# Performance work log

Measured on AMD Instinct MI355X. Metric: run time of the kernel, lower is better.

The kernel has to match this reference:

```python
import jax, jax.numpy as jnp
import numpy as np

B, K, D = 8, 1024, 512
H, DQ, DV = 8, 64, 64


def setup_inputs() -> dict:
    key = jax.random.key(0)
    ks = jax.random.split(key, 11)
    s = 0.02  # param init scale
    return {
        "query": jax.random.normal(ks[0], (B, K, D), jnp.float32),
        "key": jax.random.normal(ks[1], (B, K, D), jnp.float32),
        "value": jax.random.normal(ks[2], (B, K, D), jnp.float32),
        "Wq": jax.random.normal(ks[3], (D, H * DQ), jnp.float32) * s,
        "bq": jax.random.normal(ks[4], (H * DQ,), jnp.float32) * s,
        "Wk": jax.random.normal(ks[5], (D, H * DQ), jnp.float32) * s,
        "bk": jax.random.normal(ks[6], (H * DQ,), jnp.float32) * s,
        "Wv": jax.random.normal(ks[7], (D, H * DV), jnp.float32) * s,
        "bv": jax.random.normal(ks[8], (H * DV,), jnp.float32) * s,
        "Wo": jax.random.normal(ks[9], (H * DV, D), jnp.float32) * s,
        "bo": jax.random.normal(ks[10], (D,), jnp.float32) * s,
    }


def reference(query, key, value, Wq, bq, Wk, bk, Wv, bv, Wo, bo):
    b, k, _ = query.shape
    # Linear projections, split into heads: chunk(h, dim=-1) + cat(dim=0)
    # is equivalent to reshape (b, k, h, d) with head on a separate axis.
    q = (query @ Wq + bq).reshape(b, k, H, DQ)  # b k h dq
    kk = (key @ Wk + bk).reshape(b, k, H, DQ)   # b k h dq
    v = (value @ Wv + bv).reshape(b, k, H, DV)  # b k h dv
    # NOTE: original scales by sqrt(K) (sequence length), not sqrt(dq).
    scale = 1.0 / jnp.sqrt(jnp.asarray(k, q.dtype))
    scores = jnp.einsum("bqhd,bkhd->bhqk", q, kk) * scale
    attn = jax.nn.softmax(scores, axis=-1)
    ctx = jnp.einsum("bhqk,bkhd->bqhd", attn, v).reshape(b, k, H * DV)
    return ctx @ Wo + bo
```

## Files before the change

### kernel.cpp

```cpp
#include <hip/hip_runtime.h>
#include <hip/hip_bf16.h>

#define DEVI __device__ __forceinline__

typedef __attribute__((ext_vector_type(4))) float f32x4;
typedef __attribute__((ext_vector_type(8))) short bf16x8;

static constexpr int BB  = 8;
static constexpr int SEQ = 1024;
static constexpr int DIM = 512;
static constexpr int NH  = 8;
static constexpr int HD  = 64;
static constexpr int M   = BB * SEQ;


DEVI unsigned short f2bf(float x) {
  unsigned int u = __builtin_bit_cast(unsigned int, x);
  u += 0x7fffu + ((u >> 16) & 1u);
  return (unsigned short)(u >> 16);
}

DEVI float fexp2(float x) {
#if __has_builtin(__builtin_amdgcn_exp2f)
  return __builtin_amdgcn_exp2f(x);
#else
  float r; asm("v_exp_f32 %0, %1" : "=v"(r) : "v"(x)); return r;
#endif
}

DEVI void gload_lds16(const unsigned short* g, unsigned short* l) {
  __builtin_amdgcn_global_load_lds(
      (const __attribute__((address_space(1))) void*)g,
      (__attribute__((address_space(3))) void*)l, 16, 0, 0);
}


__global__ __launch_bounds__(256) void cvt3_kernel(const float* __restrict__ a,
                                                   const float* __restrict__ b,
                                                   const float* __restrict__ c,
                                                   unsigned short* __restrict__ oa,
                                                   unsigned short* __restrict__ ob,
                                                   unsigned short* __restrict__ oc) {
  const float* in = (blockIdx.y == 0) ? a : ((blockIdx.y == 1) ? b : c);
  unsigned short* out = (blockIdx.y == 0) ? oa : ((blockIdx.y == 1) ? ob : oc);
  int i = (blockIdx.x * 256 + threadIdx.x) * 4;
  float4 v = *reinterpret_cast<const float4*>(in + i);
  ushort4 o;
  o.x = f2bf(v.x); o.y = f2bf(v.y); o.z = f2bf(v.z); o.w = f2bf(v.w);
  *reinterpret_cast<ushort4*>(out + i) = o;
}


__global__ __launch_bounds__(256) void cvt_t4_kernel(const float* __restrict__ w0,
                                                     const float* __restrict__ w1,
                                                     const float* __restrict__ w2,
                                                     const float* __restrict__ w3,
                                                     unsigned short* __restrict__ o0,
                                                     unsigned short* __restrict__ o1,
                                                     unsigned short* __restrict__ o2,
                                                     unsigned short* __restrict__ o3) {
  const float* in = (blockIdx.z == 0) ? w0 : ((blockIdx.z == 1) ? w1 : ((blockIdx.z == 2) ? w2 : w3));
  unsigned short* out = (blockIdx.z == 0) ? o0 : ((blockIdx.z == 1) ? o1 : ((blockIdx.z == 2) ? o2 : o3));
  __shared__ float tile[32][33];
  int n0 = blockIdx.x * 32, k0 = blockIdx.y * 32;
  int tx = threadIdx.x & 31, ty = threadIdx.x >> 5;
#pragma unroll
  for (int r = 0; r < 32; r += 8)
    tile[ty + r][tx] = in[(size_t)(k0 + ty + r) * DIM + n0 + tx];
  __syncthreads();
#pragma unroll
  for (int r = 0; r < 32; r += 8)
    out[(size_t)(n0 + ty + r) * DIM + k0 + tx] = f2bf(tile[tx][ty + r]);
}


__global__ __launch_bounds__(256) void gemm_proj(const unsigned short* __restrict__ Aq,
                                                 const unsigned short* __restrict__ Ak,
                                                 const unsigned short* __restrict__ Av,
                                                 const unsigned short* __restrict__ WqT,
                                                 const unsigned short* __restrict__ WkT,
                                                 const unsigned short* __restrict__ WvT,
                                                 const float* __restrict__ bq,
                                                 const float* __restrict__ bk,
                                                 const float* __restrict__ bv,
                                                 unsigned short* __restrict__ qb,
                                                 unsigned short* __restrict__ kb,
                                                 unsigned short* __restrict__ vT,
                                                 float qscale) {
  __shared__ unsigned short smem[17408];
  unsigned short* lA = smem;
  unsigned short* lB = smem + 8192;

  const int z = blockIdx.z;
  const unsigned short* A = (z == 0) ? Aq : ((z == 1) ? Ak : Av);
  const unsigned short* Bt = (z == 0) ? WqT : ((z == 1) ? WkT : WvT);
  const float* bias = (z == 0) ? bq : ((z == 1) ? bk : bv);
  const float gs = (z == 0) ? qscale : 1.0f;

  const int tid = threadIdx.x;
  const int lane = tid & 63, wave = tid >> 6;
  const int wr = wave >> 1, wc = wave & 1;
  const int row0 = blockIdx.x * 128, col0 = blockIdx.y * 128;
  const int lr = lane & 15, lg = lane >> 4;

  f32x4 acc[4][4] = {};

  const int s0a = wave * 64;
  const int sA = s0a + lane, rA = sA >> 2, koA = (sA & 3) * 8;
  const int s0b = 256 + wave * 64;
  const int sB = s0b + lane, rB = sB >> 2, koB = (sB & 3) * 8;

#define GEMM_STAGE(buf, k0)                                                              \
  do {                                                                                   \
    gload_lds16(A + (size_t)(row0 + rA) * DIM + (k0) + koA, &lA[(buf)*4096 + s0a * 8]);  \
    gload_lds16(Bt + (size_t)(col0 + rA) * DIM + (k0) + koA, &lB[(buf)*4096 + s0a * 8]); \
    gload_lds16(A + (size_t)(row0 + rB) * DIM + (k0) + koB, &lA[(buf)*4096 + s0b * 8]);  \
    gload_lds16(Bt + (size_t)(col0 + rB) * DIM + (k0) + koB, &lB[(buf)*4096 + s0b * 8]); \
  } while (0)

  GEMM_STAGE(0, 0);
  __syncthreads();

  constexpr int NT = DIM / 32;
  for (int t = 0; t < NT; ++t) {
    const int cur = t & 1;
    if (t + 1 < NT) GEMM_STAGE(cur ^ 1, (t + 1) * 32);

    bf16x8 af[4], bfr[4];
#pragma unroll
    for (int m = 0; m < 4; ++m)
      af[m] = *reinterpret_cast<const bf16x8*>(&lA[cur * 4096 + (wr * 64 + m * 16 + lr) * 32 + lg * 8]);
#pragma unroll
    for (int n = 0; n < 4; ++n)
      bfr[n] = *reinterpret_cast<const bf16x8*>(&lB[cur * 4096 + (wc * 64 + n * 16 + lr) * 32 + lg * 8]);
    __builtin_amdgcn_s_setprio(1);
#pragma unroll
    for (int m = 0; m < 4; ++m)
#pragma unroll
      for (int n = 0; n < 4; ++n)
        acc[m][n] = __builtin_amdgcn_mfma_f32_16x16x32_bf16(af[m], bfr[n], acc[m][n], 0, 0, 0);
    __builtin_amdgcn_s_setprio(0);

    __syncthreads();
  }
#undef GEMM_STAGE

  if (z < 2) {
    unsigned short* C = (z == 0) ? qb : kb;
#pragma unroll
    for (int m = 0; m < 4; ++m) {
#pragma unroll
      for (int n = 0; n < 4; ++n) {
        int col = col0 + wc * 64 + n * 16 + lr;
        int r0 = row0 + wr * 64 + m * 16 + lg * 4;
        float bvv = bias[col];
#pragma unroll
        for (int j = 0; j < 4; ++j)
          C[(size_t)(r0 + j) * DIM + col] = f2bf((acc[m][n][j] + bvv) * gs);
      }
    }
  } else {
    unsigned short* ldsT = smem;
#pragma unroll
    for (int m = 0; m < 4; ++m) {
#pragma unroll
      for (int n = 0; n < 4; ++n) {
        const int col = wc * 64 + n * 16 + lr;
        const int r0l = wr * 64 + m * 16 + lg * 4;
        const float bvv = bias[col0 + col];
        ushort4 pk;
        pk.x = f2bf(acc[m][n][0] + bvv);
        pk.y = f2bf(acc[m][n][1] + bvv);
        pk.z = f2bf(acc[m][n][2] + bvv);
        pk.w = f2bf(acc[m][n][3] + bvv);
        *reinterpret_cast<ushort4*>(&ldsT[col * 136 + r0l]) = pk;
      }
    }
    __syncthreads();
    const int b = row0 >> 10, s_loc0 = row0 & 1023;
#pragma unroll
    for (int it = 0; it < 8; ++it) {
      int idx = it * 256 + tid;
      int c = idx >> 4, s8 = idx & 15;
      bf16x8 v = *reinterpret_cast<const bf16x8*>(&ldsT[c * 136 + s8 * 8]);
      *reinterpret_cast<bf16x8*>(
          vT + ((size_t)(b * DIM) + col0 + c) * SEQ + s_loc0 + s8 * 8) = v;
    }
  }
}


__global__ __launch_bounds__(256) void gemm_out(const unsigned short* __restrict__ A,
                                                const unsigned short* __restrict__ Bt,
                                                const float* __restrict__ bias,
                                                float* __restrict__ C) {
  __shared__ unsigned short lA[2][128 * 32];
  __shared__ unsigned short lB[2][128 * 32];
  const int tid = threadIdx.x;
  const int lane = tid & 63, wave = tid >> 6;
  const int wr = wave >> 1, wc = wave & 1;
  const int row0 = blockIdx.x * 128, col0 = blockIdx.y * 128;
  const int lr = lane & 15, lg = lane >> 4;

  f32x4 acc[4][4] = {};

  const int s0a = wave * 64;
  const int sA = s0a + lane, rA = sA >> 2, koA = (sA & 3) * 8;
  const int s0b = 256 + wave * 64;
  const int sB = s0b + lane, rB = sB >> 2, koB = (sB & 3) * 8;

#define GEMM_STAGE(buf, k0)                                                        \
  do {                                                                             \
    gload_lds16(A + (size_t)(row0 + rA) * DIM + (k0) + koA, &lA[buf][s0a * 8]);    \
    gload_lds16(Bt + (size_t)(col0 + rA) * DIM + (k0) + koA, &lB[buf][s0a * 8]);   \
    gload_lds16(A + (size_t)(row0 + rB) * DIM + (k0) + koB, &lA[buf][s0b * 8]);    \
    gload_lds16(Bt + (size_t)(col0 + rB) * DIM + (k0) + koB, &lB[buf][s0b * 8]);   \
  } while (0)

  GEMM_STAGE(0, 0);
  __syncthreads();

  constexpr int NT = DIM / 32;
  for (int t = 0; t < NT; ++t) {
    const int cur = t & 1;
    if (t + 1 < NT) GEMM_STAGE(cur ^ 1, (t + 1) * 32);

    bf16x8 af[4], bfr[4];
#pragma unroll
    for (int m = 0; m < 4; ++m)
      af[m] = *reinterpret_cast<const bf16x8*>(&lA[cur][(wr * 64 + m * 16 + lr) * 32 + lg * 8]);
#pragma unroll
    for (int n = 0; n < 4; ++n)
      bfr[n] = *reinterpret_cast<const bf16x8*>(&lB[cur][(wc * 64 + n * 16 + lr) * 32 + lg * 8]);
    __builtin_amdgcn_s_setprio(1);
#pragma unroll
    for (int m = 0; m < 4; ++m)
#pragma unroll
      for (int n = 0; n < 4; ++n)
        acc[m][n] = __builtin_amdgcn_mfma_f32_16x16x32_bf16(af[m], bfr[n], acc[m][n], 0, 0, 0);
    __builtin_amdgcn_s_setprio(0);

    __syncthreads();
  }
#undef GEMM_STAGE

#pragma unroll
  for (int m = 0; m < 4; ++m) {
#pragma unroll
    for (int n = 0; n < 4; ++n) {
      int col = col0 + wc * 64 + n * 16 + lr;
      int r0 = row0 + wr * 64 + m * 16 + lg * 4;
      float bv = bias[col];
#pragma unroll
      for (int j = 0; j < 4; ++j)
        C[(size_t)(r0 + j) * DIM + col] = acc[m][n][j] + bv;
    }
  }
}


__global__ __launch_bounds__(512) void attn_kernel(const unsigned short* __restrict__ qb,
                                                   const unsigned short* __restrict__ kb,
                                                   const unsigned short* __restrict__ vT,
                                                   unsigned short* __restrict__ ctx) {
  __shared__ unsigned short lK[2][64 * 64];
  __shared__ unsigned short lV[2][64 * 64];
  __shared__ unsigned short Pl[8][16 * 72];

  const int b = blockIdx.z, h = blockIdx.y;
  const int tid = threadIdx.x, lane = tid & 63, wave = tid >> 6;
  const int lr = lane & 15, lg = lane >> 4;
  const int q0 = blockIdx.x * 128 + wave * 16;

  const int sr = tid >> 3, sc = (tid & 7) ^ (sr & 7);
  const unsigned short* Kbase = kb + ((size_t)b * SEQ) * DIM + (size_t)h * HD;
  const unsigned short* Vbase = vT + (size_t)(b * NH + h) * HD * SEQ;

  bf16x8 qf0, qf1;
  {
    const unsigned short* qrow = qb + ((size_t)(b * SEQ) + q0 + lr) * DIM + h * HD;
    qf0 = *reinterpret_cast<const bf16x8*>(qrow + lg * 8);
    qf1 = *reinterpret_cast<const bf16x8*>(qrow + 32 + lg * 8);
  }

  float l_r[4] = {0.f, 0.f, 0.f, 0.f};
  f32x4 o_acc[4];
#pragma unroll
  for (int n = 0; n < 4; ++n) o_acc[n] = f32x4{0.f, 0.f, 0.f, 0.f};

  unsigned short* pw = Pl[wave];

  gload_lds16(Kbase + (size_t)sr * DIM + sc * 8, &lK[0][(wave * 64) * 8]);
  gload_lds16(Vbase + (size_t)sr * SEQ + sc * 8, &lV[0][(wave * 64) * 8]);
  __syncthreads();

  for (int t = 0; t < SEQ / 64; ++t) {
    const int cur = t & 1;
    if (t + 1 < SEQ / 64) {
      const int nk = (t + 1) * 64;
      gload_lds16(Kbase + (size_t)(nk + sr) * DIM + sc * 8, &lK[cur ^ 1][(wave * 64) * 8]);
      gload_lds16(Vbase + (size_t)sr * SEQ + nk + sc * 8, &lV[cur ^ 1][(wave * 64) * 8]);
    }

    f32x4 st[4];
    __builtin_amdgcn_s_setprio(1);
#pragma unroll
    for (int kt = 0; kt < 4; ++kt) {
      const int row = kt * 16 + lr;
      const char* rbase = (const char*)&lK[cur][0] + row * 128;
      const int sw = (row & 7) << 4;
      bf16x8 kf0 = *reinterpret_cast<const bf16x8*>(rbase + ((lg * 16) ^ sw));
      bf16x8 kf1 = *reinterpret_cast<const bf16x8*>(rbase + ((64 + lg * 16) ^ sw));
      f32x4 a = {};
      a = __builtin_amdgcn_mfma_f32_16x16x32_bf16(qf0, kf0, a, 0, 0, 0);
      a = __builtin_amdgcn_mfma_f32_16x16x32_bf16(qf1, kf1, a, 0, 0, 0);
      st[kt] = a;
    }
    __builtin_amdgcn_s_setprio(0);

#pragma unroll
    for (int j = 0; j < 4; ++j) {
      float p0 = fexp2(st[0][j]);
      float p1 = fexp2(st[1][j]);
      float p2 = fexp2(st[2][j]);
      float p3 = fexp2(st[3][j]);
      l_r[j] += (p0 + p1) + (p2 + p3);
      const int qrow = (lg * 4 + j) * 72;
      pw[qrow + lr] = f2bf(p0);
      pw[qrow + 16 + lr] = f2bf(p1);
      pw[qrow + 32 + lr] = f2bf(p2);
      pw[qrow + 48 + lr] = f2bf(p3);
    }

#pragma unroll
    for (int c = 0; c < 2; ++c) {
      bf16x8 pf = *reinterpret_cast<const bf16x8*>((const char*)pw + lr * 144 + c * 64 + lg * 16);
      __builtin_amdgcn_s_setprio(1);
#pragma unroll
      for (int n = 0; n < 4; ++n) {
        const int row = n * 16 + lr;
        bf16x8 vf = *reinterpret_cast<const bf16x8*>(
            (const char*)&lV[cur][0] + row * 128 + ((c * 64 + lg * 16) ^ ((row & 7) << 4)));
        o_acc[n] = __builtin_amdgcn_mfma_f32_16x16x32_bf16(pf, vf, o_acc[n], 0, 0, 0);
      }
      __builtin_amdgcn_s_setprio(0);
    }

    __syncthreads();
  }

  float invl[4];
#pragma unroll
  for (int j = 0; j < 4; ++j) {
    float l = l_r[j];
#pragma unroll
    for (int msk = 1; msk < 16; msk <<= 1) l += __shfl_xor(l, msk);
    invl[j] = 1.f / l;
  }
#pragma unroll
  for (int n = 0; n < 4; ++n)
#pragma unroll
    for (int j = 0; j < 4; ++j)
      pw[(lg * 4 + j) * 72 + n * 16 + lr] = f2bf(o_acc[n][j] * invl[j]);

#pragma unroll
  for (int it = 0; it < 2; ++it) {
    int idx = it * 64 + lane;
    int r = idx >> 3, cc = idx & 7;
    bf16x8 v = *reinterpret_cast<const bf16x8*>((const char*)pw + r * 144 + cc * 16);
    *reinterpret_cast<bf16x8*>(ctx + ((size_t)(b * SEQ) + q0 + r) * DIM + h * HD + cc * 8) = v;
  }
}


extern "C" void kernel_launch(void* const* d_in, const int* in_sizes, int n_in,
                              void* d_out, int out_size, void* d_ws, size_t ws_size,
                              hipStream_t stream) {
  const float* query = (const float*)d_in[0];
  const float* key_  = (const float*)d_in[1];
  const float* value = (const float*)d_in[2];
  const float* Wq = (const float*)d_in[3];
  const float* bq = (const float*)d_in[4];
  const float* Wk = (const float*)d_in[5];
  const float* bk = (const float*)d_in[6];
  const float* Wv = (const float*)d_in[7];
  const float* bv = (const float*)d_in[8];
  const float* Wo = (const float*)d_in[9];
  const float* bo = (const float*)d_in[10];
  float* out = (float*)d_out;

  unsigned short* ws = (unsigned short*)d_ws;
  const size_t NM = (size_t)M * DIM;
  const size_t NW = (size_t)DIM * DIM;
  unsigned short* xq   = ws;
  unsigned short* xk   = xq + NM;
  unsigned short* xv   = xk + NM;
  unsigned short* qb   = xv + NM;
  unsigned short* kbuf = qb + NM;
  unsigned short* vTb  = kbuf + NM;
  unsigned short* ctx  = vTb + NM;
  unsigned short* Wqt  = ctx + NM;
  unsigned short* Wkt  = Wqt + NW;
  unsigned short* Wvt  = Wkt + NW;
  unsigned short* Wot  = Wvt + NW;

  cvt3_kernel<<<dim3((int)(NM / 1024), 3), 256, 0, stream>>>(query, key_, value, xq, xk, xv);
  cvt_t4_kernel<<<dim3(16, 16, 4), 256, 0, stream>>>(Wq, Wk, Wv, Wo, Wqt, Wkt, Wvt, Wot);

  const float qscale = 0.03125f * 1.4426950408889634f;
  gemm_proj<<<dim3(M / 128, DIM / 128, 3), 256, 0, stream>>>(
      xq, xk, xv, Wqt, Wkt, Wvt, bq, bk, bv, qb, kbuf, vTb, qscale);

  attn_kernel<<<dim3(SEQ / 128, NH, BB), 512, 0, stream>>>(qb, kbuf, vTb, ctx);

  gemm_out<<<dim3(M / 128, DIM / 128), 256, 0, stream>>>(ctx, Wot, bo, out);
}
```

Before: 86.22 us.

## Triple-buffer LDS tiles in projection and output GEMMs with explicit vmcnt waits

Both GEMM kernels move from double-buffered to triple-buffered LDS staging. Loads run two k-tiles ahead, and explicit s_waitcnt vmcnt counts replace the full __syncthreads drain. The intent is to hide more global-load latency behind MFMA work. In exchange each block uses more shared memory, which may lower occupancy, and each step now has two barriers.

New measurement: 81.37 us. 1.06x faster.

```diff
diff --git a/kernel.cpp b/kernel.cpp
--- a/kernel.cpp
+++ b/kernel.cpp
@@ -87,9 +87,9 @@
                                                  unsigned short* __restrict__ kb,
                                                  unsigned short* __restrict__ vT,
                                                  float qscale) {
-  __shared__ unsigned short smem[17408];
+  __shared__ unsigned short smem[24576];
   unsigned short* lA = smem;
-  unsigned short* lB = smem + 8192;
+  unsigned short* lB = smem + 12288;
 
   const int z = blockIdx.z;
   const unsigned short* A = (z == 0) ? Aq : ((z == 1) ? Ak : Av);
@@ -118,32 +118,39 @@
     gload_lds16(Bt + (size_t)(col0 + rB) * DIM + (k0) + koB, &lB[(buf)*4096 + s0b * 8]); \
   } while (0)
 
+#define GEMM_STEP(cur, VMC)                                                              \
+  do {                                                                                   \
+    asm volatile("s_waitcnt vmcnt(" #VMC ")" ::: "memory");                              \
+    __builtin_amdgcn_s_barrier();                                                        \
+    bf16x8 af[4], bfr[4];                                                                \
+    _Pragma("unroll")                                                                    \
+    for (int m = 0; m < 4; ++m)                                                          \
+      af[m] = *reinterpret_cast<const bf16x8*>(&lA[(cur)*4096 + (wr * 64 + m * 16 + lr) * 32 + lg * 8]); \
+    _Pragma("unroll")                                                                    \
+    for (int n = 0; n < 4; ++n)                                                          \
+      bfr[n] = *reinterpret_cast<const bf16x8*>(&lB[(cur)*4096 + (wc * 64 + n * 16 + lr) * 32 + lg * 8]); \
+    __builtin_amdgcn_s_setprio(1);                                                       \
+    _Pragma("unroll")                                                                    \
+    for (int m = 0; m < 4; ++m)                                                          \
+      _Pragma("unroll")                                                                  \
+      for (int n = 0; n < 4; ++n)                                                        \
+        acc[m][n] = __builtin_amdgcn_mfma_f32_16x16x32_bf16(af[m], bfr[n], acc[m][n], 0, 0, 0); \
+    __builtin_amdgcn_s_setprio(0);                                                       \
+    asm volatile("" ::: "memory");                                                       \
+    __builtin_amdgcn_s_barrier();                                                        \
+  } while (0)
+
+  constexpr int NT = DIM / 32;
   GEMM_STAGE(0, 0);
-  __syncthreads();
-
-  constexpr int NT = DIM / 32;
-  for (int t = 0; t < NT; ++t) {
-    const int cur = t & 1;
-    if (t + 1 < NT) GEMM_STAGE(cur ^ 1, (t + 1) * 32);
-
-    bf16x8 af[4], bfr[4];
-#pragma unroll
-    for (int m = 0; m < 4; ++m)
-      af[m] = *reinterpret_cast<const bf16x8*>(&lA[cur * 4096 + (wr * 64 + m * 16 + lr) * 32 + lg * 8]);
-#pragma unroll
-    for (int n = 0; n < 4; ++n)
-      bfr[n] = *reinterpret_cast<const bf16x8*>(&lB[cur * 4096 + (wc * 64 + n * 16 + lr) * 32 + lg * 8]);
-    __builtin_amdgcn_s_setprio(1);
-#pragma unroll
-    for (int m = 0; m < 4; ++m)
-#pragma unroll
-      for (int n = 0; n < 4; ++n)
-        acc[m][n] = __builtin_amdgcn_mfma_f32_16x16x32_bf16(af[m], bfr[n], acc[m][n], 0, 0, 0);
-    __builtin_amdgcn_s_setprio(0);
-
-    __syncthreads();
-  }
+  GEMM_STAGE(1, 32);
+  for (int t = 0; t < NT - 2; ++t) {
+    GEMM_STAGE((t + 2) % 3, (t + 2) * 32);
+    GEMM_STEP(t % 3, 8);
+  }
+  GEMM_STEP((NT - 2) % 3, 4);
+  GEMM_STEP((NT - 1) % 3, 0);
 #undef GEMM_STAGE
+#undef GEMM_STEP
 
   if (z < 2) {
     unsigned short* C = (z == 0) ? qb : kb;
@@ -161,6 +168,7 @@
     }
   } else {
     unsigned short* ldsT = smem;
+    __syncthreads();
 #pragma unroll
     for (int m = 0; m < 4; ++m) {
 #pragma unroll
@@ -194,8 +202,8 @@
                                                 const unsigned short* __restrict__ Bt,
                                                 const float* __restrict__ bias,
                                                 float* __restrict__ C) {
-  __shared__ unsigned short lA[2][128 * 32];
-  __shared__ unsigned short lB[2][128 * 32];
+  __shared__ unsigned short lA[3][128 * 32];
+  __shared__ unsigned short lB[3][128 * 32];
   const int tid = threadIdx.x;
   const int lane = tid & 63, wave = tid >> 6;
   const int wr = wave >> 1, wc = wave & 1;
@@ -217,32 +225,39 @@
     gload_lds16(Bt + (size_t)(col0 + rB) * DIM + (k0) + koB, &lB[buf][s0b * 8]);   \
   } while (0)
 
+#define GEMM_STEP(cur, VMC)                                                        \
+  do {                                                                             \
+    asm volatile("s_waitcnt vmcnt(" #VMC ")" ::: "memory");                        \
+    __builtin_amdgcn_s_barrier();                                                  \
+    bf16x8 af[4], bfr[4];                                                          \
+    _Pragma("unroll")                                                              \
+    for (int m = 0; m < 4; ++m)                                                    \
+      af[m] = *reinterpret_cast<const bf16x8*>(&lA[cur][(wr * 64 + m * 16 + lr) * 32 + lg * 8]); \
+    _Pragma("unroll")                                                              \
+    for (int n = 0; n < 4; ++n)                                                    \
+      bfr[n] = *reinterpret_cast<const bf16x8*>(&lB[cur][(wc * 64 + n * 16 + lr) * 32 + lg * 8]); \
+    __builtin_amdgcn_s_setprio(1);                                                 \
+    _Pragma("unroll")                                                              \
+    for (int m = 0; m < 4; ++m)                                                    \
+      _Pragma("unroll")                                                            \
+      for (int n = 0; n < 4; ++n)                                                  \
+        acc[m][n] = __builtin_amdgcn_mfma_f32_16x16x32_bf16(af[m], bfr[n], acc[m][n], 0, 0, 0); \
+    __builtin_amdgcn_s_setprio(0);                                                 \
+    asm volatile("" ::: "memory");                                                 \
+    __builtin_amdgcn_s_barrier();                                                  \
+  } while (0)
+
+  constexpr int NT = DIM / 32;
   GEMM_STAGE(0, 0);
-  __syncthreads();
-
-  constexpr int NT = DIM / 32;
-  for (int t = 0; t < NT; ++t) {
-    const int cur = t & 1;
-    if (t + 1 < NT) GEMM_STAGE(cur ^ 1, (t + 1) * 32);
-
-    bf16x8 af[4], bfr[4];
-#pragma unroll
-    for (int m = 0; m < 4; ++m)
-      af[m] = *reinterpret_cast<const bf16x8*>(&lA[cur][(wr * 64 + m * 16 + lr) * 32 + lg * 8]);
-#pragma unroll
-    for (int n = 0; n < 4; ++n)
-      bfr[n] = *reinterpret_cast<const bf16x8*>(&lB[cur][(wc * 64 + n * 16 + lr) * 32 + lg * 8]);
-    __builtin_amdgcn_s_setprio(1);
-#pragma unroll
-    for (int m = 0; m < 4; ++m)
-#pragma unroll
-      for (int n = 0; n < 4; ++n)
-        acc[m][n] = __builtin_amdgcn_mfma_f32_16x16x32_bf16(af[m], bfr[n], acc[m][n], 0, 0, 0);
-    __builtin_amdgcn_s_setprio(0);
-
-    __syncthreads();
-  }
+  GEMM_STAGE(1, 32);
+  for (int t = 0; t < NT - 2; ++t) {
+    GEMM_STAGE((t + 2) % 3, (t + 2) * 32);
+    GEMM_STEP((t % 3), 8);
+  }
+  GEMM_STEP(((NT - 2) % 3), 4);
+  GEMM_STEP(((NT - 1) % 3), 0);
 #undef GEMM_STAGE
+#undef GEMM_STEP
 
 #pragma unroll
   for (int m = 0; m < 4; ++m) {
```
